# Optimization experiments

Hardware: AMD Instinct MI355X
Metric: run time of the kernel (lower is better)

Reference implementation:

```python
import jax, jax.numpy as jnp
import numpy as np

START_TAG = 7
STOP_TAG = 8
NEG = -10000.0  # matches torch.full((1,K), -10000.) in the original


def setup_inputs() -> dict:
    key = jax.random.key(0)
    k1, k2, k3, k4 = jax.random.split(key, 4)
    B, T, K = 1024, 2048, 9  # K = output_dim + 2 (START/STOP hardcoded as 7/8)
    feats = jax.random.normal(k1, (B, T, K), dtype=jnp.float32)
    tags = jax.random.randint(k2, (B, T), 0, 7)            # valid labels 0..6
    lengths = jax.random.randint(k3, (B,), 1, T + 1)        # per-sentence lengths >= 1
    transitions = jax.random.normal(k4, (K, K), dtype=jnp.float32)
    transitions = transitions.at[START_TAG, :].set(NEG)     # never transition into START
    transitions = transitions.at[:, STOP_TAG].set(NEG)      # never transition out of STOP
    return {"feats": feats, "transitions": transitions, "tags": tags, "lengths": lengths}


def _crf_nll(feats, transitions, tags, lengths):
    # feats: [B,T,K] emissions, transitions[j,i] = score of i -> j
    B, T, K = feats.shape

    def fwd_one(feat, length):
        # CRF forward algorithm (log partition), vectorized over tags,
        # lax.scan over time; masked past `length` to emulate feats[:x_len].
        alpha0 = jnp.full((K,), NEG, feat.dtype).at[START_TAG].set(0.0)

        def step(alpha, inp):
            t, f = inp
            # alpha_new[j] = logsumexp_i(alpha[i] + transitions[j,i]) + feat[t,j]
            new = jax.nn.logsumexp(alpha[None, :] + transitions, axis=1) + f
            return jnp.where(t < length, new, alpha), None

        alpha, _ = jax.lax.scan(step, alpha0, (jnp.arange(T), feat))
        return jax.nn.logsumexp(alpha + transitions[STOP_TAG])

    fwd_scores = jax.vmap(fwd_one)(feats, lengths)  # [B]

    def gold_one(feat, tg, length):
        # _score_sentence: sum_t trans[tags[t], tags[t-1]] + feat[t, tags[t]]
        prev = jnp.concatenate([jnp.array([START_TAG], tg.dtype), tg[:-1]])
        step_scores = transitions[tg, prev] + jnp.take_along_axis(feat, tg[:, None], axis=1)[:, 0]
        mask = jnp.arange(tg.shape[0]) < length
        last = tg[length - 1]
        return jnp.sum(jnp.where(mask, step_scores, 0.0)) + transitions[STOP_TAG, last]

    gold_scores = jax.vmap(gold_one)(feats, tags, lengths)  # [B]

    # neg_log_likelihood accumulates (forward - gold) per sentence, then / n
    return jnp.mean(fwd_scores - gold_scores)


def reference(feats, transitions, tags, lengths):
    return _crf_nll(feats, transitions, tags, lengths)
```

## Files before the change

### kernel.cpp

```cpp
#include <hip/hip_runtime.h>


#define START_TAG 7
#define STOP_TAG  8
#define KD     9
#define NS     7
#define CHUNKS 32
#define SLOT   56
#define NEG1   (-1e30f)

__device__ __forceinline__ float rfl(float x) {
    return __int_as_float(__builtin_amdgcn_readfirstlane(__float_as_int(x)));
}

__global__ __launch_bounds__(64, 3) void crf_chunkA(
    const float* __restrict__ feats,
    const float* __restrict__ trans,
    const int*   __restrict__ lengths,
    float* __restrict__ logM,
    int T, int L)
{
    float E[49];
    #pragma unroll
    for (int k = 0; k < 49; ++k)
        E[k] = rfl(__expf(trans[(k / 7) * KD + (k % 7)]));

    const int gtid  = blockIdx.x * 64 + threadIdx.x;
    const int lane8 = gtid & 7;
    const int grp   = gtid >> 3;
    const int c     = grp & (CHUNKS - 1);
    const int b     = grp >> 5;

    const int len    = lengths[b];
    const int t0     = c * L;
    const int tstart = (t0 > 1) ? t0 : 1;
    const int tend   = min(t0 + L, len);
    const int n      = tend - tstart;
    if (lane8 >= NS || n <= 0) return;

    const float* fp = feats + ((size_t)b * T + tstart) * KD;

    float p[NS];
    #pragma unroll
    for (int j = 0; j < NS; ++j) p[j] = (j == lane8) ? 1.f : 0.f;
    float s = 0.f;

    const int mb   = n >> 2;
    const int tail = n & 3;
    const int nm1  = n - 1;

    float4 B0[8], B1[8], B2[8];

    #define LOADB(DST, M) do {                                                  \
        int r0_ = min(4*(M)+0, nm1), r1_ = min(4*(M)+1, nm1);                   \
        int r2_ = min(4*(M)+2, nm1), r3_ = min(4*(M)+3, nm1);                   \
        DST[0] = *(const float4*)(fp + r0_*KD); DST[1] = *(const float4*)(fp + r0_*KD + 4); \
        DST[2] = *(const float4*)(fp + r1_*KD); DST[3] = *(const float4*)(fp + r1_*KD + 4); \
        DST[4] = *(const float4*)(fp + r2_*KD); DST[5] = *(const float4*)(fp + r2_*KD + 4); \
        DST[6] = *(const float4*)(fp + r3_*KD); DST[7] = *(const float4*)(fp + r3_*KD + 4); \
    } while (0)

    #define STEP(FA, FB) do {                                                   \
        float ef[NS] = { __expf((FA).x), __expf((FA).y), __expf((FA).z),        \
                         __expf((FA).w), __expf((FB).x), __expf((FB).y),        \
                         __expf((FB).z) };                                      \
        float q[NS];                                                            \
        _Pragma("unroll")                                                       \
        for (int j = 0; j < NS; ++j) {                                          \
            float acc = E[j*7] * p[0];                                          \
            _Pragma("unroll")                                                   \
            for (int i = 1; i < NS; ++i) acc = fmaf(E[j*7+i], p[i], acc);       \
            q[j] = acc;                                                         \
        }                                                                       \
        _Pragma("unroll")                                                       \
        for (int j = 0; j < NS; ++j) p[j] = q[j] * ef[j];                       \
    } while (0)

    #define RENORM() do {                                                       \
        float m = p[0];                                                         \
        _Pragma("unroll")                                                       \
        for (int j = 1; j < NS; ++j) m = fmaxf(m, p[j]);                        \
        float rm = __builtin_amdgcn_rcpf(m);                                    \
        _Pragma("unroll")                                                       \
        for (int j = 0; j < NS; ++j) p[j] *= rm;                                \
        s += __logf(m);                                                         \
    } while (0)

    LOADB(B0, 0);
    LOADB(B1, 1);

    for (int m = 0; m < mb; ++m) {
        LOADB(B2, m + 2);
        STEP(B0[0], B0[1]); STEP(B0[2], B0[3]);
        STEP(B0[4], B0[5]); STEP(B0[6], B0[7]);
        RENORM();
        #pragma unroll
        for (int k = 0; k < 8; ++k) { B0[k] = B1[k]; B1[k] = B2[k]; }
    }
    if (tail > 0) {
        STEP(B0[0], B0[1]);
        if (tail > 1) STEP(B0[2], B0[3]);
        if (tail > 2) STEP(B0[4], B0[5]);
        RENORM();
    }

    float* outp = logM + (size_t)grp * SLOT + lane8 * 8;
    #pragma unroll
    for (int j = 0; j < NS; ++j)
        outp[j] = fmaxf(__logf(p[j]), NEG1) + s;

    #undef LOADB
    #undef STEP
    #undef RENORM
}

__global__ __launch_bounds__(256) void crf_combineB(
    const float* __restrict__ feats,
    const float* __restrict__ trans,
    const int*   __restrict__ tags,
    const int*   __restrict__ lengths,
    const float* __restrict__ logM,
    float* __restrict__ perb,
    int T, int L)
{
    __shared__ float s_trans[81];
    __shared__ float s_mat[CHUNKS * 64];
    __shared__ float s_buf[(CHUNKS / 2) * 64];
    __shared__ float s_gold[4];
    __shared__ float s_alpha0[8];

    const int tid = threadIdx.x;
    const int b   = blockIdx.x;
    const int len = lengths[b];
    const float* fbase = feats + (size_t)b * T * KD;
    const int*   tg    = tags  + (size_t)b * T;

    if (tid < 81) s_trans[tid] = trans[tid];
    __syncthreads();

    {
        int per = (T >> 8) > 0 ? (T >> 8) : 1;
        int t0  = tid * per;
        float g = 0.f;
        if (t0 < len) {
            int te   = min(t0 + per, len);
            int prev = (t0 == 0) ? START_TAG : tg[t0 - 1];
            for (int k = 0; k < per; ++k) {
                int t   = t0 + k;
                int tc  = min(t, te - 1);
                int cur = tg[tc];
                float v = s_trans[cur * KD + prev] + fbase[(size_t)tc * KD + cur];
                g += (t < te) ? v : 0.f;
                prev = cur;
            }
            if (len - 1 >= t0 && len - 1 < t0 + per)
                g += s_trans[STOP_TAG * KD + tg[len - 1]];
        }
        #pragma unroll
        for (int off = 32; off > 0; off >>= 1) g += __shfl_xor(g, off, 64);
        if ((tid & 63) == 0) s_gold[tid >> 6] = g;
    }

    if (tid < 8)
        s_alpha0[tid] = (tid < NS) ? (s_trans[tid * KD + START_TAG] + fbase[tid]) : NEG1;

    for (int idx = tid; idx < CHUNKS * SLOT; idx += 256) {
        int c = idx / SLOT, k = idx - c * SLOT;
        bool act = (c == 0) ? (len > 1) : (c * L < len);
        float v;
        if (act) v = logM[(size_t)(b * CHUNKS + c) * SLOT + k];
        else     v = ((k >> 3) == (k & 7)) ? 0.f : NEG1;
        s_mat[c * 64 + k] = v;
    }
    __syncthreads();

    const int  e    = tid >> 6;
    const int  lane = tid & 63;
    const int  j    = lane % 7;
    const int  i    = lane / 7;
    const bool actl = lane < 49;

    #define PRODROUND(SRC, DST, P) do {                                         \
        for (int p_ = e; p_ < (P); p_ += 4) {                                   \
            const float* Lb = (SRC) + (2 * p_ + 1) * 64;                        \
            const float* Rb = (SRC) + (2 * p_) * 64;                            \
            if (actl) {                                                         \
                float tv[NS];                                                   \
                tv[0] = Lb[j] + Rb[i * 8];                                      \
                float tm = tv[0];                                               \
                _Pragma("unroll")                                               \
                for (int k = 1; k < NS; ++k) {                                  \
                    tv[k] = Lb[k * 8 + j] + Rb[i * 8 + k];                      \
                    tm = fmaxf(tm, tv[k]);                                      \
                }                                                               \
                float sum = 0.f;                                                \
                _Pragma("unroll")                                               \
                for (int k = 0; k < NS; ++k) sum += __expf(tv[k] - tm);         \
                (DST)[p_ * 64 + i * 8 + j] = tm + __logf(sum);                  \
            }                                                                   \
        }                                                                       \
        __syncthreads();                                                        \
    } while (0)

    PRODROUND(s_mat, s_buf, 16);
    PRODROUND(s_buf, s_mat, 8);
    PRODROUND(s_mat, s_buf, 4);
    PRODROUND(s_buf, s_mat, 2);
    PRODROUND(s_mat, s_buf, 1);
    #undef PRODROUND

    if (tid < 8) {
        const bool isrow = (tid < NS);
        const int  jj    = isrow ? tid : 0;
        float tv[NS];
        tv[0] = s_buf[jj] + s_alpha0[0];
        float tm = tv[0];
        #pragma unroll
        for (int i2 = 1; i2 < NS; ++i2) {
            tv[i2] = s_buf[i2 * 8 + jj] + s_alpha0[i2];
            tm = fmaxf(tm, tv[i2]);
        }
        float sum = 0.f;
        #pragma unroll
        for (int i2 = 0; i2 < NS; ++i2) sum += __expf(tv[i2] - tm);
        float af = tm + __logf(sum);

        float term = isrow ? (af + s_trans[STOP_TAG * KD + tid]) : NEG1;
        float tm2 = term;
        #pragma unroll
        for (int off = 4; off > 0; off >>= 1) tm2 = fmaxf(tm2, __shfl_xor(tm2, off, 8));
        float ee = isrow ? __expf(term - tm2) : 0.f;
        #pragma unroll
        for (int off = 4; off > 0; off >>= 1) ee += __shfl_xor(ee, off, 8);

        if (tid == 0) {
            float fwd = tm2 + __logf(ee);
            perb[b] = fwd - (s_gold[0] + s_gold[1] + s_gold[2] + s_gold[3]);
        }
    }
}

__global__ __launch_bounds__(256) void crf_reduceC(
    const float* __restrict__ perb, float* __restrict__ out, int B)
{
    __shared__ float sd[256];
    float s = 0.f;
    for (int i = threadIdx.x; i < B; i += 256) s += perb[i];
    sd[threadIdx.x] = s;
    __syncthreads();
    for (int st = 128; st > 0; st >>= 1) {
        if (threadIdx.x < st) sd[threadIdx.x] += sd[threadIdx.x + st];
        __syncthreads();
    }
    if (threadIdx.x == 0) out[0] = sd[0] / (float)B;
}

extern "C" void kernel_launch(void* const* d_in, const int* in_sizes, int n_in,
                              void* d_out, int out_size, void* d_ws, size_t ws_size,
                              hipStream_t stream) {
    const float* feats   = (const float*)d_in[0];
    const float* trans   = (const float*)d_in[1];
    const int*   tags    = (const int*)d_in[2];
    const int*   lengths = (const int*)d_in[3];

    int B = in_sizes[3];
    int T = in_sizes[2] / B;
    int L = (T + CHUNKS - 1) / CHUNKS;

    float* logM = (float*)d_ws;
    float* perb = logM + (size_t)B * CHUNKS * SLOT;

    crf_chunkA<<<(B * CHUNKS * 8) / 64, 64, 0, stream>>>(
        feats, trans, lengths, logM, T, L);
    crf_combineB<<<B, 256, 0, stream>>>(
        feats, trans, tags, lengths, logM, perb, T, L);
    crf_reduceC<<<1, 256, 0, stream>>>(perb, (float*)d_out, B);
}
```

Baseline: 164.6 us.

## Double chunk count, pack logM slots, and double-buffer feature loads

Splits each sentence into 64 time chunks instead of 32, doubling thread-level parallelism in the chunk kernel while shortening each sequential chain, and adds one more log-semiring tree-reduction round in the combine kernel. The per-chunk transfer matrix is packed to 49 floats instead of a padded 56. Feature loads switch from a triple-buffer copy rotation to ping-pong double buffering, occupancy is raised to 4 blocks per SIMD, and renormalization accumulates in log2. The extra chunks cost more logM traffic and more combine work per sentence.

```diff
diff --git a/kernel.cpp b/kernel.cpp
--- a/kernel.cpp
+++ b/kernel.cpp
@@ -5,15 +5,16 @@
 #define STOP_TAG  8
 #define KD     9
 #define NS     7
-#define CHUNKS 32
-#define SLOT   56
+#define CHUNKS 64
+#define SLOT   49
 #define NEG1   (-1e30f)
+#define LN2F   0.69314718056f
 
 __device__ __forceinline__ float rfl(float x) {
     return __int_as_float(__builtin_amdgcn_readfirstlane(__float_as_int(x)));
 }
 
-__global__ __launch_bounds__(64, 3) void crf_chunkA(
+__global__ __launch_bounds__(64, 4) void crf_chunkA(
     const float* __restrict__ feats,
     const float* __restrict__ trans,
     const int*   __restrict__ lengths,
@@ -29,7 +30,7 @@
     const int lane8 = gtid & 7;
     const int grp   = gtid >> 3;
     const int c     = grp & (CHUNKS - 1);
-    const int b     = grp >> 5;
+    const int b     = grp >> 6;
 
     const int len    = lengths[b];
     const int t0     = c * L;
@@ -43,13 +44,13 @@
     float p[NS];
     #pragma unroll
     for (int j = 0; j < NS; ++j) p[j] = (j == lane8) ? 1.f : 0.f;
-    float s = 0.f;
+    float s2 = 0.f;
 
     const int mb   = n >> 2;
     const int tail = n & 3;
     const int nm1  = n - 1;
 
-    float4 B0[8], B1[8], B2[8];
+    float4 A0[8], A1[8];
 
     #define LOADB(DST, M) do {                                                  \
         int r0_ = min(4*(M)+0, nm1), r1_ = min(4*(M)+1, nm1);                   \
@@ -76,6 +77,11 @@
         for (int j = 0; j < NS; ++j) p[j] = q[j] * ef[j];                       \
     } while (0)
 
+    #define STEP4(BUF) do {                                                     \
+        STEP(BUF[0], BUF[1]); STEP(BUF[2], BUF[3]);                             \
+        STEP(BUF[4], BUF[5]); STEP(BUF[6], BUF[7]);                             \
+    } while (0)
+
     #define RENORM() do {                                                       \
         float m = p[0];                                                         \
         _Pragma("unroll")                                                       \
@@ -83,34 +89,44 @@
         float rm = __builtin_amdgcn_rcpf(m);                                    \
         _Pragma("unroll")                                                       \
         for (int j = 0; j < NS; ++j) p[j] *= rm;                                \
-        s += __logf(m);                                                         \
-    } while (0)
-
-    LOADB(B0, 0);
-    LOADB(B1, 1);
-
-    for (int m = 0; m < mb; ++m) {
-        LOADB(B2, m + 2);
-        STEP(B0[0], B0[1]); STEP(B0[2], B0[3]);
-        STEP(B0[4], B0[5]); STEP(B0[6], B0[7]);
-        RENORM();
-        #pragma unroll
-        for (int k = 0; k < 8; ++k) { B0[k] = B1[k]; B1[k] = B2[k]; }
-    }
-    if (tail > 0) {
-        STEP(B0[0], B0[1]);
-        if (tail > 1) STEP(B0[2], B0[3]);
-        if (tail > 2) STEP(B0[4], B0[5]);
-        RENORM();
-    }
-
-    float* outp = logM + (size_t)grp * SLOT + lane8 * 8;
+        s2 += __log2f(m);                                                       \
+    } while (0)
+
+    LOADB(A0, 0);
+
+    int m = 0;
+    for (; m + 2 <= mb; m += 2) {
+        LOADB(A1, m + 1);
+        STEP4(A0); RENORM();
+        LOADB(A0, m + 2);
+        STEP4(A1); RENORM();
+    }
+    if (m < mb) {
+        LOADB(A1, m + 1);
+        STEP4(A0); RENORM();
+        if (tail > 0) {
+            STEP(A1[0], A1[1]);
+            if (tail > 1) STEP(A1[2], A1[3]);
+            if (tail > 2) STEP(A1[4], A1[5]);
+            RENORM();
+        }
+    } else {
+        if (tail > 0) {
+            STEP(A0[0], A0[1]);
+            if (tail > 1) STEP(A0[2], A0[3]);
+            if (tail > 2) STEP(A0[4], A0[5]);
+            RENORM();
+        }
+    }
+
+    float* outp = logM + (size_t)grp * SLOT + lane8 * 7;
     #pragma unroll
     for (int j = 0; j < NS; ++j)
-        outp[j] = fmaxf(__logf(p[j]), NEG1) + s;
+        outp[j] = fmaxf((__log2f(p[j]) + s2) * LN2F, NEG1);
 
     #undef LOADB
     #undef STEP
+    #undef STEP4
     #undef RENORM
 }
 
@@ -166,11 +182,12 @@
 
     for (int idx = tid; idx < CHUNKS * SLOT; idx += 256) {
         int c = idx / SLOT, k = idx - c * SLOT;
+        int i = k / 7, j = k - i * 7;
         bool act = (c == 0) ? (len > 1) : (c * L < len);
         float v;
         if (act) v = logM[(size_t)(b * CHUNKS + c) * SLOT + k];
-        else     v = ((k >> 3) == (k & 7)) ? 0.f : NEG1;
-        s_mat[c * 64 + k] = v;
+        else     v = (i == j) ? 0.f : NEG1;
+        s_mat[c * 64 + i * 8 + j] = v;
     }
     __syncthreads();
 
@@ -202,22 +219,23 @@
         __syncthreads();                                                        \
     } while (0)
 
-    PRODROUND(s_mat, s_buf, 16);
-    PRODROUND(s_buf, s_mat, 8);
-    PRODROUND(s_mat, s_buf, 4);
-    PRODROUND(s_buf, s_mat, 2);
-    PRODROUND(s_mat, s_buf, 1);
+    PRODROUND(s_mat, s_buf, 32);
+    PRODROUND(s_buf, s_mat, 16);
+    PRODROUND(s_mat, s_buf, 8);
+    PRODROUND(s_buf, s_mat, 4);
+    PRODROUND(s_mat, s_buf, 2);
+    PRODROUND(s_buf, s_mat, 1);
     #undef PRODROUND
 
     if (tid < 8) {
         const bool isrow = (tid < NS);
         const int  jj    = isrow ? tid : 0;
         float tv[NS];
-        tv[0] = s_buf[jj] + s_alpha0[0];
+        tv[0] = s_mat[jj] + s_alpha0[0];
         float tm = tv[0];
         #pragma unroll
         for (int i2 = 1; i2 < NS; ++i2) {
-            tv[i2] = s_buf[i2 * 8 + jj] + s_alpha0[i2];
+            tv[i2] = s_mat[i2 * 8 + jj] + s_alpha0[i2];
             tm = fmaxf(tm, tv[i2]);
         }
         float sum = 0.f;
```

Result: slower. 177.8 us (+8.0%).
